# Kernel optimization log

Hardware: AMD Instinct MI355X
Metric: run time of the kernel (lower is better)

The kernel has to match this reference:

```python
import jax, jax.numpy as jnp
import numpy as np

N = 50000       # nodes
E = 800000      # edges (avg degree 16)
C_IN = 128
C_OUT = 128
H = 4           # attention heads
D = C_OUT // H  # per-head dim
G = 8           # group-norm groups
NEG_SLOPE_ACT = 0.01   # nn.LeakyReLU() default
NEG_SLOPE_ATT = 0.2    # GAT attention LeakyReLU slope


def _glorot(key, shape):
    fan = shape[0] + (shape[-1] if len(shape) > 1 else shape[0])
    lim = np.sqrt(6.0 / fan).astype(np.float32)
    return jax.random.uniform(key, shape, jnp.float32, -lim, lim)


def setup_inputs() -> dict:
    key = jax.random.key(0)
    ks = jax.random.split(key, 8)
    inp = {
        "x": jax.random.normal(ks[0], (N, C_IN), jnp.float32),
        "edge_index": jax.random.randint(ks[1], (2, E), 0, N),
        "edge_weight": jax.random.uniform(ks[2], (E,), jnp.float32),
    }
    dims = [C_IN, C_OUT]
    for l in range(2):
        cin = dims[l]
        k = jax.random.split(ks[3 + l], 8)
        inp[f"gamma{l}"] = jnp.ones((cin,), jnp.float32)
        inp[f"beta{l}"] = jnp.zeros((cin,), jnp.float32)
        inp[f"W{l}"] = _glorot(k[0], (cin, H * D))
        inp[f"We{l}"] = _glorot(k[1], (1, H * D))
        inp[f"a_src{l}"] = _glorot(k[2], (H, D))
        inp[f"a_dst{l}"] = _glorot(k[3], (H, D))
        inp[f"a_edge{l}"] = _glorot(k[4], (H, D))
        inp[f"bias{l}"] = jnp.zeros((H * D,), jnp.float32)
    return inp


def group_norm(x, gamma, beta, eps=1e-5):
    n, c = x.shape
    xg = x.reshape(n, G, c // G)
    mu = xg.mean(-1, keepdims=True)
    var = xg.var(-1, keepdims=True)
    xn = ((xg - mu) * jax.lax.rsqrt(var + eps)).reshape(n, c)
    return xn * gamma + beta


def gat_layer(x, src, dst, ew, W, We, a_src, a_dst, a_edge, bias):
    h = (x @ W).reshape(N, H, D)                   # [N,H,D]
    he = (ew[:, None] @ We).reshape(-1, H, D)      # [E',H,D] edge-weight embedding
    logits = ((h * a_src).sum(-1)[src]
              + (h * a_dst).sum(-1)[dst]
              + (he * a_edge).sum(-1))             # [E',H]
    logits = jax.nn.leaky_relu(logits, NEG_SLOPE_ATT)
    m = jax.ops.segment_max(logits, dst, num_segments=N)
    m = jax.lax.stop_gradient(jnp.where(jnp.isfinite(m), m, 0.0))
    e = jnp.exp(logits - m[dst])
    s = jax.ops.segment_sum(e, dst, num_segments=N)
    alpha = e / (s[dst] + 1e-16)                   # softmax over in-edges per dst, per head
    out = jax.ops.segment_sum(alpha[:, :, None] * h[src], dst, num_segments=N)
    return out.reshape(N, H * D) + bias


def reference(x, edge_index, edge_weight,
              gamma0, beta0, W0, We0, a_src0, a_dst0, a_edge0, bias0,
              gamma1, beta1, W1, We1, a_src1, a_dst1, a_edge1, bias1):
    loop = jnp.arange(N)
    src = jnp.concatenate([edge_index[0], loop])
    dst = jnp.concatenate([edge_index[1], loop])
    # self-loop fill_value='max': self edges get the max edge weight
    ew = jnp.concatenate([edge_weight, jnp.full((N,), edge_weight.max())])
    params = [(gamma0, beta0, W0, We0, a_src0, a_dst0, a_edge0, bias0),
              (gamma1, beta1, W1, We1, a_src1, a_dst1, a_edge1, bias1)]
    for g, b, W, We, asrc, adst, ae, bias in params:
        x = group_norm(x, g, b)
        x = jax.nn.leaky_relu(x, NEG_SLOPE_ACT)
        x = gat_layer(x, src, dst, ew, W, We, asrc, adst, ae, bias)
    return x
```

## Files before the change

kernel.cpp:

```cpp
#include <hip/hip_runtime.h>
#include <hip/hip_bf16.h>
#include <math.h>

#define CN 128
#define NBLK 256
#define BSH 8

typedef __attribute__((ext_vector_type(8))) short bf16x8;
typedef __attribute__((ext_vector_type(4))) float f32x4;

static __device__ inline unsigned int pack_bf16x2(float lo, float hi) {
    unsigned int ul = __float_as_uint(lo);
    unsigned int uh = __float_as_uint(hi);
    ul = (ul + 0x7fffu + ((ul >> 16) & 1u)) >> 16;
    uh = (uh + 0x7fffu + ((uh >> 16) & 1u)) & 0xffff0000u;
    return ul | uh;
}
static __device__ inline unsigned short bf16_of(float v) {
    unsigned int u = __float_as_uint(v);
    return (unsigned short)((u + 0x7fffu + ((u >> 16) & 1u)) >> 16);
}

__global__ __launch_bounds__(256) void kbA(const int* __restrict__ dsts,
                                           const float* __restrict__ ew,
                                           int e, int n,
                                           int* __restrict__ hist,
                                           int* __restrict__ ewmaxArr,
                                           const float* __restrict__ W0,
                                           const float* __restrict__ W1,
                                           const float* __restrict__ We0,
                                           const float* __restrict__ ae0,
                                           const float* __restrict__ We1,
                                           const float* __restrict__ ae1,
                                           unsigned short* __restrict__ wt0,
                                           unsigned short* __restrict__ wt1,
                                           float* __restrict__ ce) {
    __shared__ int lh[256];
    __shared__ int wm[4];
    int t = threadIdx.x, blk = blockIdx.x;
    if (blk >= NBLK) {
        int b = blk - NBLK;
        if (b < 2) {
            const float* W = b ? W1 : W0;
            unsigned short* wt = b ? wt1 : wt0;
            for (int i = t; i < CN * CN; i += 256) {
                int k = i >> 7, c = i & 127;
                wt[c * CN + k] = bf16_of(W[k * CN + c]);
            }
        } else if (t < 8) {
            const float* We = (t < 4) ? We0 : We1;
            const float* ae = (t < 4) ? ae0 : ae1;
            int h = t & 3;
            float s = 0.f;
            for (int d = 0; d < 32; d++) s += We[h * 32 + d] * ae[h * 32 + d];
            ce[t] = s;
        }
        return;
    }
    lh[t] = 0;
    __syncthreads();
    int tot = e + n;
    int chunk = (tot + NBLK - 1) / NBLK;
    int start = blk * chunk, end = min(start + chunk, tot);
    float m = 0.f;
    for (int i = start + t; i < end; i += 256) {
        int d;
        if (i < e) { d = dsts[i]; m = fmaxf(m, ew[i]); }
        else       { d = i - e; }
        atomicAdd(&lh[d >> BSH], 1);
    }
#pragma unroll
    for (int off = 1; off < 64; off <<= 1) m = fmaxf(m, __shfl_xor(m, off));
    if ((t & 63) == 0) wm[t >> 6] = __float_as_int(m);
    __syncthreads();
    hist[t * NBLK + blk] = lh[t];
    if (t == 0)
        ewmaxArr[blk] = max(max(wm[0], wm[1]), max(wm[2], wm[3]));
}

__global__ __launch_bounds__(256) void kscanL(int* __restrict__ a,
                                              int* __restrict__ bsum) {
    __shared__ int wsum[4];
    int t = threadIdx.x, blk = blockIdx.x;
    int idx = blk * 256 + t;
    int v = a[idx];
    int s = v;
    int lane = t & 63, wid = t >> 6;
#pragma unroll
    for (int off = 1; off < 64; off <<= 1) {
        int u = __shfl_up(s, off);
        if (lane >= off) s += u;
    }
    if (lane == 63) wsum[wid] = s;
    __syncthreads();
    int add = 0;
#pragma unroll
    for (int w = 0; w < 4; w++) if (w < wid) add += wsum[w];
    s += add;
    a[idx] = s - v;
    if (t == 255) bsum[blk] = s;
}

__global__ __launch_bounds__(256) void kbB(const int* __restrict__ srcs,
                                           const int* __restrict__ dsts,
                                           const float* __restrict__ ew,
                                           const int* __restrict__ ewmaxArr,
                                           const int* __restrict__ hsc,
                                           const int* __restrict__ bsum,
                                           int2* __restrict__ inter, int e, int n) {
    __shared__ int cur[256];
    __shared__ int wsum[4];
    __shared__ int wmI;
    int t = threadIdx.x, blk = blockIdx.x;
    if (t == 0) wmI = 0;
    int v = bsum[t];
    int s = v;
    int lane = t & 63, wid = t >> 6;
#pragma unroll
    for (int off = 1; off < 64; off <<= 1) {
        int u = __shfl_up(s, off);
        if (lane >= off) s += u;
    }
    int mi = ewmaxArr[t];
#pragma unroll
    for (int off = 1; off < 64; off <<= 1) mi = max(mi, __shfl_xor(mi, off));
    if (lane == 63) wsum[wid] = s;
    __syncthreads();
    int add = 0;
#pragma unroll
    for (int w = 0; w < 4; w++) if (w < wid) add += wsum[w];
    s += add;
    cur[t] = hsc[t * NBLK + blk] + (s - v);
    if (lane == 0) atomicMax(&wmI, mi);
    __syncthreads();
    float wmax = __int_as_float(wmI);
    int tot = e + n;
    int chunk = (tot + NBLK - 1) / NBLK;
    int start = blk * chunk, end = min(start + chunk, tot);
    for (int i = start + t; i < end; i += 256) {
        int sn, d; float w;
        if (i < e) { sn = srcs[i]; d = dsts[i]; w = ew[i]; }
        else       { sn = i - e;   d = sn;      w = wmax;  }
        int p = atomicAdd(&cur[d >> BSH], 1);
        inter[p] = make_int2((d << 16) | sn, __float_as_int(w));
    }
}

static __device__ void kbc_body(int* cnt, int* cur, int* wsum, int* bexc,
                                int b,
                                const int* __restrict__ hsc,
                                const int* __restrict__ bsum,
                                const int2* __restrict__ inter,
                                unsigned int* __restrict__ edges,
                                int* __restrict__ rowptr,
                                int n, int nb, int ep) {
    int t = threadIdx.x;
    int lane = t & 63, wid = t >> 6;
    {
        int v = bsum[t];
        int s = v;
#pragma unroll
        for (int off = 1; off < 64; off <<= 1) {
            int u = __shfl_up(s, off);
            if (lane >= off) s += u;
        }
        if (lane == 63) wsum[wid] = s;
        __syncthreads();
        int add = 0;
#pragma unroll
        for (int w = 0; w < 4; w++) if (w < wid) add += wsum[w];
        s += add;
        bexc[t] = s - v;
        if (t == 255) bexc[256] = s;
    }
    cnt[t] = 0;
    __syncthreads();
    int rstart = hsc[b * NBLK] + bexc[b];
    int rend = (b + 1 < 256) ? (hsc[(b + 1) * NBLK] + bexc[b + 1]) : ep;
    for (int i = rstart + t; i < rend; i += 256)
        atomicAdd(&cnt[(inter[i].x >> 16) & 255], 1);
    __syncthreads();
    int v = cnt[t];
    int s = v;
#pragma unroll
    for (int off = 1; off < 64; off <<= 1) {
        int u = __shfl_up(s, off);
        if (lane >= off) s += u;
    }
    if (lane == 63) wsum[wid] = s;
    __syncthreads();
    int wexcl = 0;
#pragma unroll
    for (int w = 0; w < 4; w++) if (w < wid) wexcl += wsum[w];
    int excl = wexcl + s - v;
    int node = (b << BSH) + t;
    int gpos = rstart + excl;
    if (node < n) rowptr[node] = gpos;
    if (b == nb - 1 && t == 0) rowptr[n] = ep;
    cur[t] = gpos;
    __syncthreads();
    for (int i = rstart + t; i < rend; i += 256) {
        int2 r = inter[i];
        int p = atomicAdd(&cur[(r.x >> 16) & 255], 1);
        unsigned int wb = bf16_of(__int_as_float(r.y));
        edges[p] = (unsigned int)(r.x & 0xffff) | (wb << 16);
    }
}

static __device__ void kgn_body(short* xs, int block_row,
                                const float* __restrict__ xin,
                                const uint4* __restrict__ xin_b,
                                int inbf16, const float* __restrict__ gamma,
                                const float* __restrict__ beta,
                                const unsigned short* __restrict__ wt,
                                const float* __restrict__ asrc,
                                const float* __restrict__ adst,
                                unsigned int* __restrict__ hout,
                                float* __restrict__ ssrc,
                                float* __restrict__ sdst, int n) {
    int t = threadIdx.x;
    int lane = t & 63, w = t >> 6;
    int m = lane & 15, quad = lane >> 4;

    {
        int r = t & 63;
        int row = block_row + r;
        uint4* dst = (uint4*)xs;
#pragma unroll
        for (int u2 = 0; u2 < 2; u2++) {
            int g = (t >> 6) * 2 + u2;
            uint4 lo, hi;
            if (row < n) {
                float v[16];
                if (inbf16) {
                    uint4 A = xin_b[(size_t)row * 16 + g * 2];
                    uint4 B = xin_b[(size_t)row * 16 + g * 2 + 1];
                    unsigned int uu[8] = {A.x,A.y,A.z,A.w,B.x,B.y,B.z,B.w};
#pragma unroll
                    for (int j = 0; j < 8; j++) {
                        v[2*j]   = __uint_as_float(uu[j] << 16);
                        v[2*j+1] = __uint_as_float(uu[j] & 0xffff0000u);
                    }
                } else {
                    const float4* xr = (const float4*)(xin + (size_t)row * CN + g * 16);
                    float4 A = xr[0], B = xr[1], C = xr[2], D = xr[3];
                    float tmp[16] = {A.x,A.y,A.z,A.w,B.x,B.y,B.z,B.w,
                                     C.x,C.y,C.z,C.w,D.x,D.y,D.z,D.w};
#pragma unroll
                    for (int j = 0; j < 16; j++) v[j] = tmp[j];
                }
                float mu = 0.f;
#pragma unroll
                for (int j = 0; j < 16; j++) mu += v[j];
                mu *= 0.0625f;
                float var = 0.f;
#pragma unroll
                for (int j = 0; j < 16; j++) { float d2 = v[j] - mu; var += d2 * d2; }
                var *= 0.0625f;
                float rsv = rsqrtf(var + 1e-5f);
                const float4* gp = (const float4*)(gamma + g * 16);
                const float4* bp = (const float4*)(beta + g * 16);
                float4 g0 = gp[0], g1 = gp[1], g2 = gp[2], g3 = gp[3];
                float4 b0 = bp[0], b1 = bp[1], b2 = bp[2], b3 = bp[3];
                float gv[16] = {g0.x,g0.y,g0.z,g0.w,g1.x,g1.y,g1.z,g1.w,
                                g2.x,g2.y,g2.z,g2.w,g3.x,g3.y,g3.z,g3.w};
                float bv[16] = {b0.x,b0.y,b0.z,b0.w,b1.x,b1.y,b1.z,b1.w,
                                b2.x,b2.y,b2.z,b2.w,b3.x,b3.y,b3.z,b3.w};
                float xn[16];
#pragma unroll
                for (int j = 0; j < 16; j++) {
                    float xv = (v[j] - mu) * rsv * gv[j] + bv[j];
                    xn[j] = xv > 0.f ? xv : 0.01f * xv;
                }
                lo = make_uint4(pack_bf16x2(xn[0], xn[1]),  pack_bf16x2(xn[2], xn[3]),
                                pack_bf16x2(xn[4], xn[5]),  pack_bf16x2(xn[6], xn[7]));
                hi = make_uint4(pack_bf16x2(xn[8], xn[9]),  pack_bf16x2(xn[10], xn[11]),
                                pack_bf16x2(xn[12], xn[13]), pack_bf16x2(xn[14], xn[15]));
            } else {
                lo = make_uint4(0, 0, 0, 0);
                hi = lo;
            }
            dst[r * 16 + ((2 * g)     ^ (r & 15))] = lo;
            dst[r * 16 + ((2 * g + 1) ^ (r & 15))] = hi;
        }
    }
    __syncthreads();

    f32x4 acc[4][2];
#pragma unroll
    for (int i = 0; i < 4; i++) { acc[i][0] = (f32x4)0.f; acc[i][1] = (f32x4)0.f; }

#pragma unroll
    for (int kc = 0; kc < 4; kc++) {
        int kb = 4 * kc + quad;
        bf16x8 af[4], bfr[2];
#pragma unroll
        for (int mt = 0; mt < 4; mt++)
            af[mt] = *(const bf16x8*)&xs[(16 * mt + m) * CN + ((kb ^ m) << 3)];
#pragma unroll
        for (int nt = 0; nt < 2; nt++) {
            int c = 32 * w + 16 * nt + m;
            bfr[nt] = *(const bf16x8*)&wt[c * CN + (kb << 3)];
        }
#pragma unroll
        for (int mt = 0; mt < 4; mt++) {
#pragma unroll
            for (int nt = 0; nt < 2; nt++)
                acc[mt][nt] = __builtin_amdgcn_mfma_f32_16x16x32_bf16(
                    af[mt], bfr[nt], acc[mt][nt], 0, 0, 0);
        }
    }

    float asv[2], adv[2];
#pragma unroll
    for (int nt = 0; nt < 2; nt++) {
        asv[nt] = asrc[32 * w + 16 * nt + m];
        adv[nt] = adst[32 * w + 16 * nt + m];
    }
#pragma unroll
    for (int mt = 0; mt < 4; mt++) {
#pragma unroll
        for (int j = 0; j < 4; j++) {
            float p = acc[mt][0][j] * asv[0] + acc[mt][1][j] * asv[1];
            float q = acc[mt][0][j] * adv[0] + acc[mt][1][j] * adv[1];
#pragma unroll
            for (int off = 1; off < 16; off <<= 1) {
                p += __shfl_xor(p, off);
                q += __shfl_xor(q, off);
            }
            if (m == 0) {
                int row = block_row + 16 * mt + 4 * quad + j;
                if (row < n) {
                    ssrc[row * 4 + w] = p;
                    sdst[row * 4 + w] = q;
                }
            }
        }
    }

    __syncthreads();
#pragma unroll
    for (int mt = 0; mt < 4; mt++) {
#pragma unroll
        for (int nt = 0; nt < 2; nt++) {
            int c = 32 * w + 16 * nt + m;
#pragma unroll
            for (int j = 0; j < 4; j++) {
                int rl = 16 * mt + 4 * quad + j;
                xs[rl * CN + c] = (short)bf16_of(acc[mt][nt][j]);
            }
        }
    }
    __syncthreads();
    {
        const uint4* src = (const uint4*)xs;
#pragma unroll
        for (int i = 0; i < 4; i++) {
            int u = t + 256 * i;
            int rl = u >> 4;
            int row = block_row + rl;
            if (row < n)
                *(uint4*)&hout[(size_t)row * 64 + ((u & 15) << 2)] = src[u];
        }
    }
}

__global__ __launch_bounds__(256, 4) void kbCgn(
        const int* __restrict__ hsc, const int* __restrict__ bsum,
        const int2* __restrict__ inter, unsigned int* __restrict__ edges,
        int* __restrict__ rowptr, int n, int nb, int ep,
        const float* __restrict__ xin, const float* __restrict__ gamma,
        const float* __restrict__ beta, const unsigned short* __restrict__ wt,
        const float* __restrict__ asrc, const float* __restrict__ adst,
        unsigned int* __restrict__ hout, float* __restrict__ ssrcO,
        float* __restrict__ sdstO) {
    __shared__ short xs[64 * CN];
    if ((int)blockIdx.x < nb) {
        int* cnt  = (int*)xs;
        int* cur  = (int*)(xs + 512);
        int* wsum = (int*)(xs + 1024);
        int* bexc = (int*)(xs + 2048);
        kbc_body(cnt, cur, wsum, bexc, blockIdx.x,
                 hsc, bsum, inter, edges, rowptr, n, nb, ep);
        return;
    }
    kgn_body(xs, ((int)blockIdx.x - nb) * 64, xin, (const uint4*)0, 0,
             gamma, beta, wt, asrc, adst, hout, ssrcO, sdstO, n);
}

__global__ __launch_bounds__(256, 4) void kgn_gemm7(
        const float* __restrict__ xin, const uint4* __restrict__ xin_b,
        int inbf16, const float* __restrict__ gamma,
        const float* __restrict__ beta, const unsigned short* __restrict__ wt,
        const float* __restrict__ asrc, const float* __restrict__ adst,
        unsigned int* __restrict__ hout, float* __restrict__ ssrc,
        float* __restrict__ sdst, int n) {
    __shared__ short xs[64 * CN];
    kgn_body(xs, blockIdx.x * 64, xin, xin_b, inbf16,
             gamma, beta, wt, asrc, adst, hout, ssrc, sdst, n);
}

__global__ __launch_bounds__(256, 8) void kaggr3(
        const uint4* __restrict__ h, const float* __restrict__ ssrc,
        const float* __restrict__ sdst, const int* __restrict__ rowptr,
        const unsigned int* __restrict__ edges, const float* __restrict__ ce4,
        const float* __restrict__ bias, float* __restrict__ out,
        uint4* __restrict__ outb, int packout, int n) {
    int t = threadIdx.x;
    int node = blockIdx.x * 4 + (t >> 6);
    if (node >= n) return;
    int l64 = t & 63;
    int ll = l64 & 15;
    int g  = l64 >> 4;
    int head = ll >> 2;

    int start = rowptr[node], end = rowptr[node + 1];
    float sd = sdst[node * 4 + head];
    float ce = ce4[head];

    float a0=0.f,a1=0.f,a2=0.f,a3=0.f,a4=0.f,a5=0.f,a6=0.f,a7=0.f;
    float se = 0.f;

    int i = start + g;
    for (; i + 12 < end; i += 16) {
        unsigned int er[4];
#pragma unroll
        for (int u = 0; u < 4; u++) er[u] = edges[i + 4 * u];
        float ssv[4]; uint4 U[4];
#pragma unroll
        for (int u = 0; u < 4; u++) {
            int sidx = er[u] & 0xffff;
            ssv[u] = ssrc[sidx * 4 + head];
            U[u] = h[(size_t)sidx * 16 + ll];
        }
#pragma unroll
        for (int u = 0; u < 4; u++) {
            float wv = __uint_as_float(er[u] & 0xffff0000u);
            float l = ssv[u] + sd + wv * ce;
            l = fmaxf(l, 0.2f * l);
            float e = __expf(fminf(l, 80.f));
            float h0 = __uint_as_float(U[u].x << 16);
            float h1 = __uint_as_float(U[u].x & 0xffff0000u);
            float h2 = __uint_as_float(U[u].y << 16);
            float h3 = __uint_as_float(U[u].y & 0xffff0000u);
            float h4 = __uint_as_float(U[u].z << 16);
            float h5 = __uint_as_float(U[u].z & 0xffff0000u);
            float h6 = __uint_as_float(U[u].w << 16);
            float h7 = __uint_as_float(U[u].w & 0xffff0000u);
            se += e;
            a0 = fmaf(e, h0, a0); a1 = fmaf(e, h1, a1);
            a2 = fmaf(e, h2, a2); a3 = fmaf(e, h3, a3);
            a4 = fmaf(e, h4, a4); a5 = fmaf(e, h5, a5);
            a6 = fmaf(e, h6, a6); a7 = fmaf(e, h7, a7);
        }
    }
    for (; i < end; i += 4) {
        unsigned int er = edges[i];
        int sidx = er & 0xffff;
        float ss = ssrc[sidx * 4 + head];
        uint4 U = h[(size_t)sidx * 16 + ll];
        float wv = __uint_as_float(er & 0xffff0000u);
        float l = ss + sd + wv * ce;
        l = fmaxf(l, 0.2f * l);
        float e = __expf(fminf(l, 80.f));
        float h0 = __uint_as_float(U.x << 16);
        float h1 = __uint_as_float(U.x & 0xffff0000u);
        float h2 = __uint_as_float(U.y << 16);
        float h3 = __uint_as_float(U.y & 0xffff0000u);
        float h4 = __uint_as_float(U.z << 16);
        float h5 = __uint_as_float(U.z & 0xffff0000u);
        float h6 = __uint_as_float(U.w << 16);
        float h7 = __uint_as_float(U.w & 0xffff0000u);
        se += e;
        a0 = fmaf(e, h0, a0); a1 = fmaf(e, h1, a1);
        a2 = fmaf(e, h2, a2); a3 = fmaf(e, h3, a3);
        a4 = fmaf(e, h4, a4); a5 = fmaf(e, h5, a5);
        a6 = fmaf(e, h6, a6); a7 = fmaf(e, h7, a7);
    }
#pragma unroll
    for (int off = 16; off < 64; off <<= 1) {
        a0 += __shfl_xor(a0, off); a1 += __shfl_xor(a1, off);
        a2 += __shfl_xor(a2, off); a3 += __shfl_xor(a3, off);
        a4 += __shfl_xor(a4, off); a5 += __shfl_xor(a5, off);
        a6 += __shfl_xor(a6, off); a7 += __shfl_xor(a7, off);
        se += __shfl_xor(se, off);
    }
    if (g == 0) {
        float inv = 1.f / (se + 1e-16f);
        const float4* bp = (const float4*)(bias + ll * 8);
        float4 b0 = bp[0], b1 = bp[1];
        float o0 = a0 * inv + b0.x, o1 = a1 * inv + b0.y;
        float o2 = a2 * inv + b0.z, o3 = a3 * inv + b0.w;
        float o4 = a4 * inv + b1.x, o5 = a5 * inv + b1.y;
        float o6 = a6 * inv + b1.z, o7 = a7 * inv + b1.w;
        if (packout) {
            outb[(size_t)node * 16 + ll] =
                make_uint4(pack_bf16x2(o0, o1), pack_bf16x2(o2, o3),
                           pack_bf16x2(o4, o5), pack_bf16x2(o6, o7));
        } else {
            float4* orow = (float4*)(out + (size_t)node * CN + ll * 8);
            orow[0] = make_float4(o0, o1, o2, o3);
            orow[1] = make_float4(o4, o5, o6, o7);
        }
    }
}

extern "C" void kernel_launch(void* const* d_in, const int* in_sizes, int n_in,
                              void* d_out, int out_size, void* d_ws, size_t ws_size,
                              hipStream_t stream) {
    const float* x  = (const float*)d_in[0];
    const int*   ei = (const int*)d_in[1];
    const float* ew = (const float*)d_in[2];
    int N_ = in_sizes[0] / CN;
    int E_ = in_sizes[2];
    int EP = E_ + N_;
    int NB = (N_ + 255) >> BSH;
    int NT = (N_ + 63) / 64;

    size_t off = 0;
    auto alloc = [&](size_t bytes) -> void* {
        void* p = (char*)d_ws + off;
        off += (bytes + 255) & ~(size_t)255;
        return p;
    };
    unsigned int* hbuf = (unsigned int*)alloc((size_t)N_ * 64 * 4);
    uint4* x1b     = (uint4*)alloc((size_t)N_ * 64 * 4);
    float* ssrc    = (float*)alloc((size_t)N_ * 4 * 4);
    float* sdst    = (float*)alloc((size_t)N_ * 4 * 4);
    int*   rowptr  = (int*)alloc((size_t)(N_ + 1) * 4);
    unsigned int* edges = (unsigned int*)alloc((size_t)EP * 4);
    int2*  inter   = (int2*)alloc((size_t)EP * 8);
    int*   hist    = (int*)alloc((size_t)256 * NBLK * 4);
    int*   bsum    = (int*)alloc(1024);
    int*   ewmaxArr= (int*)alloc((size_t)NBLK * 4);
    unsigned short* wt0 = (unsigned short*)alloc((size_t)CN * CN * 2);
    unsigned short* wt1 = (unsigned short*)alloc((size_t)CN * CN * 2);
    float* cedge   = (float*)alloc(256);

    const int* srcs = ei;
    const int* dsts = ei + E_;

    kbA<<<NBLK + 3, 256, 0, stream>>>(dsts, ew, E_, N_, hist, ewmaxArr,
                                      (const float*)d_in[5], (const float*)d_in[13],
                                      (const float*)d_in[6], (const float*)d_in[9],
                                      (const float*)d_in[14], (const float*)d_in[17],
                                      wt0, wt1, cedge);
    kscanL<<<256, 256, 0, stream>>>(hist, bsum);
    kbB<<<NBLK, 256, 0, stream>>>(srcs, dsts, ew, ewmaxArr, hist, bsum, inter, E_, N_);

    kbCgn<<<NB + NT, 256, 0, stream>>>(
        hist, bsum, inter, edges, rowptr, N_, NB, EP,
        x, (const float*)d_in[3], (const float*)d_in[4], wt0,
        (const float*)d_in[7], (const float*)d_in[8],
        hbuf, ssrc, sdst);

    kaggr3<<<(N_ + 3) / 4, 256, 0, stream>>>(
        (const uint4*)hbuf, ssrc, sdst, rowptr, edges, cedge,
        (const float*)d_in[10], (float*)d_out, x1b, 1, N_);

    kgn_gemm7<<<NT, 256, 0, stream>>>(
        x, (const uint4*)x1b, 1, (const float*)d_in[11], (const float*)d_in[12],
        wt1, (const float*)d_in[15], (const float*)d_in[16],
        hbuf, ssrc, sdst, N_);
    kaggr3<<<(N_ + 3) / 4, 256, 0, stream>>>(
        (const uint4*)hbuf, ssrc, sdst, rowptr, edges, cedge + 4,
        (const float*)d_in[18], (float*)d_out, x1b, 0, N_);
}
```

Before: 252.0 us.

## Fuse CSR bucket histogram and scatter into one kernel using fixed-capacity buckets

Replaces the three-kernel histogram, scan and scatter pipeline with one kernel. Each block atomically reserves space in a fixed-capacity per-bucket region of 8192 entries through global cursors, then scatters edges into it. The max edge weight is resolved later with a sentinel value, and the bucket offsets are scanned inside the CSR finalization kernel. This removes two kernel launches and one global pass over the edges. In exchange it adds a memset, assumes no bucket of 256 destination nodes exceeds 8192 edges, and makes the edge order within a bucket nondeterministic.

```diff
diff --git a/kernel.cpp b/kernel.cpp
--- a/kernel.cpp
+++ b/kernel.cpp
@@ -5,6 +5,7 @@
 #define CN 128
 #define NBLK 256
 #define BSH 8
+#define CAPSH 13
 
 typedef __attribute__((ext_vector_type(8))) short bf16x8;
 typedef __attribute__((ext_vector_type(4))) float f32x4;
@@ -21,21 +22,24 @@
     return (unsigned short)((u + 0x7fffu + ((u >> 16) & 1u)) >> 16);
 }
 
-__global__ __launch_bounds__(256) void kbA(const int* __restrict__ dsts,
-                                           const float* __restrict__ ew,
-                                           int e, int n,
-                                           int* __restrict__ hist,
-                                           int* __restrict__ ewmaxArr,
-                                           const float* __restrict__ W0,
-                                           const float* __restrict__ W1,
-                                           const float* __restrict__ We0,
-                                           const float* __restrict__ ae0,
-                                           const float* __restrict__ We1,
-                                           const float* __restrict__ ae1,
-                                           unsigned short* __restrict__ wt0,
-                                           unsigned short* __restrict__ wt1,
-                                           float* __restrict__ ce) {
+__global__ __launch_bounds__(256) void kprep(const int* __restrict__ srcs,
+                                             const int* __restrict__ dsts,
+                                             const float* __restrict__ ew,
+                                             int e, int n,
+                                             int* __restrict__ cursors,
+                                             int* __restrict__ ewmaxArr,
+                                             int2* __restrict__ inter,
+                                             const float* __restrict__ W0,
+                                             const float* __restrict__ W1,
+                                             const float* __restrict__ We0,
+                                             const float* __restrict__ ae0,
+                                             const float* __restrict__ We1,
+                                             const float* __restrict__ ae1,
+                                             unsigned short* __restrict__ wt0,
+                                             unsigned short* __restrict__ wt1,
+                                             float* __restrict__ ce) {
     __shared__ int lh[256];
+    __shared__ int cur[256];
     __shared__ int wm[4];
     int t = threadIdx.x, blk = blockIdx.x;
     if (blk >= NBLK) {
@@ -73,137 +77,84 @@
     for (int off = 1; off < 64; off <<= 1) m = fmaxf(m, __shfl_xor(m, off));
     if ((t & 63) == 0) wm[t >> 6] = __float_as_int(m);
     __syncthreads();
-    hist[t * NBLK + blk] = lh[t];
+    int c = lh[t];
+    cur[t] = c ? atomicAdd(&cursors[t * 16], c) : 0;
     if (t == 0)
         ewmaxArr[blk] = max(max(wm[0], wm[1]), max(wm[2], wm[3]));
-}
-
-__global__ __launch_bounds__(256) void kscanL(int* __restrict__ a,
-                                              int* __restrict__ bsum) {
-    __shared__ int wsum[4];
-    int t = threadIdx.x, blk = blockIdx.x;
-    int idx = blk * 256 + t;
-    int v = a[idx];
-    int s = v;
-    int lane = t & 63, wid = t >> 6;
-#pragma unroll
-    for (int off = 1; off < 64; off <<= 1) {
-        int u = __shfl_up(s, off);
-        if (lane >= off) s += u;
-    }
-    if (lane == 63) wsum[wid] = s;
-    __syncthreads();
-    int add = 0;
-#pragma unroll
-    for (int w = 0; w < 4; w++) if (w < wid) add += wsum[w];
-    s += add;
-    a[idx] = s - v;
-    if (t == 255) bsum[blk] = s;
-}
-
-__global__ __launch_bounds__(256) void kbB(const int* __restrict__ srcs,
-                                           const int* __restrict__ dsts,
-                                           const float* __restrict__ ew,
-                                           const int* __restrict__ ewmaxArr,
-                                           const int* __restrict__ hsc,
-                                           const int* __restrict__ bsum,
-                                           int2* __restrict__ inter, int e, int n) {
-    __shared__ int cur[256];
-    __shared__ int wsum[4];
-    __shared__ int wmI;
-    int t = threadIdx.x, blk = blockIdx.x;
-    if (t == 0) wmI = 0;
-    int v = bsum[t];
-    int s = v;
-    int lane = t & 63, wid = t >> 6;
-#pragma unroll
-    for (int off = 1; off < 64; off <<= 1) {
-        int u = __shfl_up(s, off);
-        if (lane >= off) s += u;
-    }
-    int mi = ewmaxArr[t];
-#pragma unroll
-    for (int off = 1; off < 64; off <<= 1) mi = max(mi, __shfl_xor(mi, off));
-    if (lane == 63) wsum[wid] = s;
-    __syncthreads();
-    int add = 0;
-#pragma unroll
-    for (int w = 0; w < 4; w++) if (w < wid) add += wsum[w];
-    s += add;
-    cur[t] = hsc[t * NBLK + blk] + (s - v);
-    if (lane == 0) atomicMax(&wmI, mi);
-    __syncthreads();
-    float wmax = __int_as_float(wmI);
-    int tot = e + n;
-    int chunk = (tot + NBLK - 1) / NBLK;
-    int start = blk * chunk, end = min(start + chunk, tot);
+    __syncthreads();
     for (int i = start + t; i < end; i += 256) {
-        int sn, d; float w;
-        if (i < e) { sn = srcs[i]; d = dsts[i]; w = ew[i]; }
-        else       { sn = i - e;   d = sn;      w = wmax;  }
-        int p = atomicAdd(&cur[d >> BSH], 1);
-        inter[p] = make_int2((d << 16) | sn, __float_as_int(w));
+        int sn, d, wbits;
+        if (i < e) { sn = srcs[i]; d = dsts[i]; wbits = __float_as_int(ew[i]); }
+        else       { sn = i - e;   d = sn;      wbits = -1; }
+        int b = d >> BSH;
+        int p = atomicAdd(&cur[b], 1);
+        inter[((size_t)b << CAPSH) + p] = make_int2((d << 16) | sn, wbits);
     }
 }
 
 static __device__ void kbc_body(int* cnt, int* cur, int* wsum, int* bexc,
-                                int b,
-                                const int* __restrict__ hsc,
-                                const int* __restrict__ bsum,
+                                int* wmI, int b,
+                                const int* __restrict__ cursors,
+                                const int* __restrict__ ewmaxArr,
                                 const int2* __restrict__ inter,
                                 unsigned int* __restrict__ edges,
                                 int* __restrict__ rowptr,
                                 int n, int nb, int ep) {
     int t = threadIdx.x;
     int lane = t & 63, wid = t >> 6;
-    {
-        int v = bsum[t];
-        int s = v;
-#pragma unroll
-        for (int off = 1; off < 64; off <<= 1) {
-            int u = __shfl_up(s, off);
-            if (lane >= off) s += u;
-        }
-        if (lane == 63) wsum[wid] = s;
-        __syncthreads();
-        int add = 0;
-#pragma unroll
-        for (int w = 0; w < 4; w++) if (w < wid) add += wsum[w];
-        s += add;
-        bexc[t] = s - v;
-        if (t == 255) bexc[256] = s;
-    }
-    cnt[t] = 0;
-    __syncthreads();
-    int rstart = hsc[b * NBLK] + bexc[b];
-    int rend = (b + 1 < 256) ? (hsc[(b + 1) * NBLK] + bexc[b + 1]) : ep;
-    for (int i = rstart + t; i < rend; i += 256)
-        atomicAdd(&cnt[(inter[i].x >> 16) & 255], 1);
-    __syncthreads();
-    int v = cnt[t];
+    if (t == 0) *wmI = 0;
+    int v = cursors[t * 16];
     int s = v;
 #pragma unroll
     for (int off = 1; off < 64; off <<= 1) {
         int u = __shfl_up(s, off);
         if (lane >= off) s += u;
     }
+    int mi = ewmaxArr[t];
+#pragma unroll
+    for (int off = 1; off < 64; off <<= 1) mi = max(mi, __shfl_xor(mi, off));
     if (lane == 63) wsum[wid] = s;
     __syncthreads();
+    if (lane == 0) atomicMax(wmI, mi);
+    int add = 0;
+#pragma unroll
+    for (int w = 0; w < 4; w++) if (w < wid) add += wsum[w];
+    s += add;
+    bexc[t] = s - v;
+    if (t == 255) bexc[256] = s;
+    cnt[t] = 0;
+    __syncthreads();
+    float wmax = __int_as_float(*wmI);
+    int cntb = cursors[b * 16];
+    size_t istart = (size_t)b << CAPSH;
+    int gbase = bexc[b];
+    for (int i = t; i < cntb; i += 256)
+        atomicAdd(&cnt[(inter[istart + i].x >> 16) & 255], 1);
+    __syncthreads();
+    int v2 = cnt[t];
+    int s2 = v2;
+#pragma unroll
+    for (int off = 1; off < 64; off <<= 1) {
+        int u = __shfl_up(s2, off);
+        if (lane >= off) s2 += u;
+    }
+    if (lane == 63) wsum[wid] = s2;
+    __syncthreads();
     int wexcl = 0;
 #pragma unroll
     for (int w = 0; w < 4; w++) if (w < wid) wexcl += wsum[w];
-    int excl = wexcl + s - v;
+    int excl = wexcl + s2 - v2;
     int node = (b << BSH) + t;
-    int gpos = rstart + excl;
+    int gpos = gbase + excl;
     if (node < n) rowptr[node] = gpos;
     if (b == nb - 1 && t == 0) rowptr[n] = ep;
     cur[t] = gpos;
     __syncthreads();
-    for (int i = rstart + t; i < rend; i += 256) {
-        int2 r = inter[i];
+    for (int i = t; i < cntb; i += 256) {
+        int2 r = inter[istart + i];
         int p = atomicAdd(&cur[(r.x >> 16) & 255], 1);
-        unsigned int wb = bf16_of(__int_as_float(r.y));
-        edges[p] = (unsigned int)(r.x & 0xffff) | (wb << 16);
+        float w = (r.y == -1) ? wmax : __int_as_float(r.y);
+        edges[p] = (unsigned int)(r.x & 0xffff) | ((unsigned int)bf16_of(w) << 16);
     }
 }
 
@@ -366,7 +317,7 @@
 }
 
 __global__ __launch_bounds__(256, 4) void kbCgn(
-        const int* __restrict__ hsc, const int* __restrict__ bsum,
+        const int* __restrict__ cursors, const int* __restrict__ ewmaxArr,
         const int2* __restrict__ inter, unsigned int* __restrict__ edges,
         int* __restrict__ rowptr, int n, int nb, int ep,
         const float* __restrict__ xin, const float* __restrict__ gamma,
@@ -379,9 +330,10 @@
         int* cnt  = (int*)xs;
         int* cur  = (int*)(xs + 512);
         int* wsum = (int*)(xs + 1024);
+        int* wmI  = (int*)(xs + 1040);
         int* bexc = (int*)(xs + 2048);
-        kbc_body(cnt, cur, wsum, bexc, blockIdx.x,
-                 hsc, bsum, inter, edges, rowptr, n, nb, ep);
+        kbc_body(cnt, cur, wsum, bexc, wmI, blockIdx.x,
+                 cursors, ewmaxArr, inter, edges, rowptr, n, nb, ep);
         return;
     }
     kgn_body(xs, ((int)blockIdx.x - nb) * 64, xin, (const uint4*)0, 0,
@@ -529,27 +481,27 @@
     float* sdst    = (float*)alloc((size_t)N_ * 4 * 4);
     int*   rowptr  = (int*)alloc((size_t)(N_ + 1) * 4);
     unsigned int* edges = (unsigned int*)alloc((size_t)EP * 4);
-    int2*  inter   = (int2*)alloc((size_t)EP * 8);
-    int*   hist    = (int*)alloc((size_t)256 * NBLK * 4);
-    int*   bsum    = (int*)alloc(1024);
+    int2*  inter   = (int2*)alloc((size_t)256 << CAPSH << 3);
+    int*   cursors = (int*)alloc((size_t)256 * 16 * 4);
     int*   ewmaxArr= (int*)alloc((size_t)NBLK * 4);
     unsigned short* wt0 = (unsigned short*)alloc((size_t)CN * CN * 2);
     unsigned short* wt1 = (unsigned short*)alloc((size_t)CN * CN * 2);
     float* cedge   = (float*)alloc(256);
 
+    hipMemsetAsync(cursors, 0, (size_t)256 * 16 * 4, stream);
+
     const int* srcs = ei;
     const int* dsts = ei + E_;
 
-    kbA<<<NBLK + 3, 256, 0, stream>>>(dsts, ew, E_, N_, hist, ewmaxArr,
-                                      (const float*)d_in[5], (const float*)d_in[13],
-                                      (const float*)d_in[6], (const float*)d_in[9],
-                                      (const float*)d_in[14], (const float*)d_in[17],
-                                      wt0, wt1, cedge);
-    kscanL<<<256, 256, 0, stream>>>(hist, bsum);
-    kbB<<<NBLK, 256, 0, stream>>>(srcs, dsts, ew, ewmaxArr, hist, bsum, inter, E_, N_);
+    kprep<<<NBLK + 3, 256, 0, stream>>>(srcs, dsts, ew, E_, N_, cursors, ewmaxArr,
+                                        inter,
+                                        (const float*)d_in[5], (const float*)d_in[13],
+                                        (const float*)d_in[6], (const float*)d_in[9],
+                                        (const float*)d_in[14], (const float*)d_in[17],
+                                        wt0, wt1, cedge);
 
     kbCgn<<<NB + NT, 256, 0, stream>>>(
-        hist, bsum, inter, edges, rowptr, N_, NB, EP,
+        cursors, ewmaxArr, inter, edges, rowptr, N_, NB, EP,
         x, (const float*)d_in[3], (const float*)d_in[4], wt0,
         (const float*)d_in[7], (const float*)d_in[8],
         hbuf, ssrc, sdst);
```

After: 247.1 us, median of 2. About the same (-1.9%).
